# Performance work log

Measured on AMD Instinct MI355X. Metric: run time of the kernel, lower is better.

Reference implementation:

```python
import jax, jax.numpy as jnp
from jax import lax
import numpy as np
import math


def make_kernel():
    # StyleGAN2 blur kernel [1,3,3,1], normalized outer product
    k = jnp.array([1.0, 3.0, 3.0, 1.0], dtype=jnp.float32)
    k2 = jnp.outer(k, k)
    return k2 / jnp.sum(k2)


def upfirdn2d(x, kernel, up=1, pad=(0, 0)):
    # x: [B,C,H,W]; depthwise FIR filter, optional zero-insert upsampling
    C = x.shape[1]
    w = jnp.tile(jnp.flip(kernel)[None, None].astype(x.dtype), (C, 1, 1, 1))
    # torch upfirdn pads up-1 trailing zeros after the last sample; lhs_dilation
    # only inserts zeros between samples, so fold the extra zeros into pad[1].
    p = (pad[0], pad[1] + up - 1)
    return lax.conv_general_dilated(
        x, w, (1, 1), (p, p), lhs_dilation=(up, up), feature_group_count=C)


def modulated_conv(x, weight, style, demodulate=True, up=False):
    # per-sample weight modulation + demodulation, executed as grouped conv
    B, Cin, H, W = x.shape
    Cout, _, k, _ = weight.shape
    scale = 1.0 / math.sqrt(Cin * k * k)
    w = scale * weight[None] * style[:, None, :, None, None]  # [B,Cout,Cin,k,k]
    if demodulate:
        d = lax.rsqrt(jnp.sum(w * w, axis=(2, 3, 4)) + 1e-8)
        w = w * d[:, :, None, None, None]
    xg = x.reshape(1, B * Cin, H, W)
    if up:
        # conv_transpose2d(stride=2, pad=0) == lhs-dilated conv with flipped kernel
        wg = jnp.flip(w, (-2, -1)).reshape(B * Cout, Cin, k, k)
        out = lax.conv_general_dilated(
            xg, wg, (1, 1), ((k - 1, k - 1), (k - 1, k - 1)),
            lhs_dilation=(2, 2), feature_group_count=B)
    else:
        pad = k // 2
        out = lax.conv_general_dilated(
            xg, w.reshape(B * Cout, Cin, k, k), (1, 1),
            ((pad, pad), (pad, pad)), feature_group_count=B)
    return out.reshape(B, Cout, out.shape[2], out.shape[3])


def fused_lrelu(x, bias):
    y = x + bias[None, :, None, None]
    return jnp.where(y >= 0, y, 0.2 * y) * math.sqrt(2.0)


def setup_inputs() -> dict:
    key = jax.random.key(0)
    ks = jax.random.split(key, 12)
    B, C, H = 8, 512, 32
    f = jnp.float32
    return {
        "x": jax.random.normal(ks[0], (B, C, H, H), f),
        "skip": jax.random.normal(ks[1], (B, 3, H, H), f),
        "w1": jax.random.normal(ks[2], (C, C, 3, 3), f),
        "b1": jnp.zeros((C,), f),
        "s1": jax.random.normal(ks[3], (B, C), f),
        "nw1": jax.random.normal(ks[4], (1,), f) * 0.1,
        "n1": jax.random.normal(ks[5], (B, 1, 2 * H, 2 * H), f),
        "w2": jax.random.normal(ks[6], (C, C, 3, 3), f),
        "b2": jnp.zeros((C,), f),
        "s2": jax.random.normal(ks[7], (B, C), f),
        "nw2": jax.random.normal(ks[8], (1,), f) * 0.1,
        "n2": jax.random.normal(ks[9], (B, 1, 2 * H, 2 * H), f),
        "w_rgb": jax.random.normal(ks[10], (3, C, 1, 1), f),
        "b_rgb": jnp.zeros((3,), f),
        "s_rgb": jax.random.normal(ks[11], (B, C), f),
    }


def reference(x, skip, w1, b1, s1, nw1, n1, w2, b2, s2, nw2, n2,
              w_rgb, b_rgb, s_rgb):
    kern = make_kernel()
    # conv1: upsampling modulated conv + blur (Blur with upsample_factor=2)
    out = modulated_conv(x, w1, s1, demodulate=True, up=True)
    out = upfirdn2d(out, kern * 4.0, up=1, pad=(1, 1))
    out = out + nw1 * n1          # NoiseInjection
    out = fused_lrelu(out, b1)    # FusedLeakyReLU
    # conv2: plain modulated conv
    out = modulated_conv(out, w2, s2, demodulate=True)
    out = out + nw2 * n2
    out = fused_lrelu(out, b2)
    # ToRGB: 1x1 mod conv, no demodulation, + bias; skip = rgb + upsample(skip)
    rgb = modulated_conv(out, w_rgb, s_rgb, demodulate=False)
    rgb = rgb + b_rgb[None, :, None, None]
    skip_up = upfirdn2d(skip, kern * 4.0, up=2, pad=(2, 1))
    return rgb + skip_up
```

## Files before the change

### kernel.cpp

```cpp
#include <hip/hip_runtime.h>
#include <stdint.h>

typedef unsigned short ushort_t;
typedef unsigned int uint_t;
typedef __bf16 bf16x8 __attribute__((ext_vector_type(8)));
typedef float f32x4 __attribute__((ext_vector_type(4)));

#define GLOBAL_AS __attribute__((address_space(1)))
#define LDS_AS    __attribute__((address_space(3)))

#define SCALE_CONV 0.014731391f
#define SCALE_RGB  0.044194174f
#define SQRT2_F    1.41421356237f

__device__ __forceinline__ void async_cp16(const void* g, void* l) {
  __builtin_amdgcn_global_load_lds((const GLOBAL_AS uint_t*)g,
                                   (LDS_AS uint_t*)l, 16, 0, 0);
}
__device__ __forceinline__ ushort_t f2bf(float v) {
  union { float f; uint_t u; } c; c.f = v;
  uint_t r = c.u + 0x7fffu + ((c.u >> 16) & 1u);
  return (ushort_t)(r >> 16);
}
__device__ __forceinline__ float bf2f(ushort_t u) {
  union { uint_t u; float f; } c; c.u = ((uint_t)u) << 16;
  return c.f;
}

__global__ __launch_bounds__(256) void prep_x1(
    const float* __restrict__ x, const float* __restrict__ s1,
    ushort_t* __restrict__ xpad) {
  __shared__ ushort_t t[32 * 520];
  const int b  = blockIdx.x >> 5;
  const int j1 = blockIdx.x & 31;
  for (int idx = threadIdx.x; idx < 512 * 32; idx += 256) {
    int ci = idx >> 5, j2 = idx & 31;
    float v = x[(size_t)(b * 512 + ci) * 1024 + j1 * 32 + j2];
    v *= s1[b * 512 + ci] * SCALE_CONV;
    t[j2 * 520 + ci] = f2bf(v);
  }
  __syncthreads();
  for (int idx = threadIdx.x; idx < 32 * 512; idx += 256) {
    int j2 = idx >> 9, ci = idx & 511;
    xpad[((size_t)(b * 34 + j1 + 1) * 34 + (j2 + 1)) * 512 + ci] = t[j2 * 520 + ci];
  }
}

__global__ __launch_bounds__(256) void prep_w(
    const float* __restrict__ w1, const float* __restrict__ w2,
    ushort_t* __restrict__ wt1, ushort_t* __restrict__ wt2,
    float* __restrict__ wsqT1, float* __restrict__ wsqT2) {
  int t = blockIdx.x * 256 + threadIdx.x;
  const float* w  = (t < 262144) ? w1 : w2;
  ushort_t*   wt  = (t < 262144) ? wt1 : wt2;
  float*      wq  = (t < 262144) ? wsqT1 : wsqT2;
  int tt = t & 262143;
  int ci = tt & 511, co = tt >> 9;
  const float* wp = w + (size_t)(co * 512 + ci) * 9;
  float sq = 0.f;
#pragma unroll
  for (int u = 0; u < 9; ++u) {
    float v = wp[u];
    sq += v * v;
    wt[((size_t)u * 512 + co) * 512 + ci] = f2bf(v);
  }
  wq[ci * 512 + co] = sq;
}

__global__ __launch_bounds__(512) void demod2(
    const float* __restrict__ wsqT1, const float* __restrict__ s1, float* __restrict__ d1,
    const float* __restrict__ wsqT2, const float* __restrict__ s2, float* __restrict__ d2) {
  const float* wq = blockIdx.y ? wsqT2 : wsqT1;
  const float* s  = blockIdx.y ? s2 : s1;
  float*       d  = blockIdx.y ? d2 : d1;
  const int b  = blockIdx.x;
  const int co = threadIdx.x;
  __shared__ float ssq[512];
  float sv = s[b * 512 + co];
  ssq[co] = sv * sv;
  __syncthreads();
  float a = 0.f;
#pragma unroll 4
  for (int ci = 0; ci < 512; ++ci) a += wq[ci * 512 + co] * ssq[ci];
  d[b * 512 + co] = rsqrtf(a * (1.f / 4608.f) + 1e-8f);
}

__global__ __launch_bounds__(256) void border_zero(
    ushort_t* __restrict__ xpad, ushort_t* __restrict__ ypad, ushort_t* __restrict__ opad) {
  const int z = blockIdx.z;
  ushort_t* p = (z == 0) ? xpad : (z == 1 ? ypad : opad);
  const int W = (z == 0) ? 34 : (z == 1 ? 67 : 66);
  const int nb = 4 * W - 4;
  const int t = blockIdx.x * 256 + threadIdx.x;
  const int pix = t >> 6, ch = (t & 63) * 8;
  if (pix >= nb) return;
  const int b = blockIdx.y;
  int y, x;
  if (pix < W)          { y = 0;     x = pix; }
  else if (pix < 2 * W) { y = W - 1; x = pix - W; }
  else { int q = pix - 2 * W; y = 1 + (q >> 1); x = (q & 1) ? W - 1 : 0; }
  uint4 z4 = {0, 0, 0, 0};
  *(uint4*)(p + ((size_t)(b * W + y) * W + x) * 512 + ch) = z4;
}

__constant__ int           c_ph_off[4]  = {0, 4, 6, 8};
__constant__ int           c_ph_ntap[4] = {4, 2, 2, 1};
__constant__ unsigned char c_tap_u1[9]  = {0,0,1,1, 0,1, 1,1, 1};
__constant__ unsigned char c_tap_u2[9]  = {0,1,0,1, 1,1, 0,1, 1};
__constant__ unsigned char c_tap_pl[9]  = {8,6,2,0, 7,1, 5,3, 4};

__global__ __launch_bounds__(256, 3) void gemm_conv1(
    const ushort_t* __restrict__ inp, const ushort_t* __restrict__ wt,
    const float* __restrict__ dmod, ushort_t* __restrict__ outp) {
  __shared__ ushort_t ldsA[128 * 64];
  __shared__ ushort_t ldsB[128 * 64];

  const int tid  = threadIdx.x;
  const int lane = tid & 63;
  const int wv   = tid >> 6;
  const int wm   = wv & 1;
  const int wn   = wv >> 1;
  const int l16  = lane & 15;
  const int quad = lane >> 4;

  const int mtile = blockIdx.x;
  const int ntile = blockIdx.y;
  const int a  = blockIdx.z;
  const int a1 = a >> 1, a2 = a & 1;

  const int cl = ((lane & 7) - (lane >> 3)) & 7;
  const char* pA[4];
  const char* pB[4];
#pragma unroll
  for (int t = 0; t < 4; ++t) {
    int row = wv * 32 + t * 8 + (lane >> 3);
    int m   = mtile * 128 + row;
    if (m > 8711) m = 8711;
    int b = m / 1089, rr = m % 1089;
    int p1 = rr / 33, p2 = rr % 33;
    size_t pix = ((size_t)(b * 34 + p1) * 34 + p2) * 512;
    pA[t] = (const char*)inp + pix * 2 + cl * 16;
    int n = ntile * 128 + row;
    pB[t] = (const char*)wt + (size_t)n * 1024 + cl * 16;
  }
  char* dstA[4];
  char* dstB[4];
#pragma unroll
  for (int t = 0; t < 4; ++t) {
    dstA[t] = (char*)ldsA + wv * 4096 + t * 1024;
    dstB[t] = (char*)ldsB + wv * 4096 + t * 1024;
  }

  int offA[4], offB[4];
#pragma unroll
  for (int i = 0; i < 4; ++i) {
    int r  = wm * 64 + i * 16 + l16;
    int rn = wn * 64 + i * 16 + l16;
    offA[i] = r  * 64 + (((quad + r)  & 7) << 3);
    offB[i] = rn * 64 + (((quad + rn) & 7) << 3);
  }

  f32x4 acc[4][4];
#pragma unroll
  for (int i = 0; i < 4; ++i)
#pragma unroll
    for (int j = 0; j < 4; ++j) acc[i][j] = (f32x4){0.f, 0.f, 0.f, 0.f};

  const int ntap = c_ph_ntap[a];
#pragma unroll 1
  for (int ti = 0; ti < ntap; ++ti) {
    int e = c_ph_off[a] + ti;
    int aoff = ((int)c_tap_u1[e] * 34 + (int)c_tap_u2[e]) * 1024;
    int boff = (int)c_tap_pl[e] * 524288;
#pragma unroll 1
    for (int kc = 0; kc < 8; ++kc) {
      const int koff = kc * 128;
      __syncthreads();
#pragma unroll
      for (int t = 0; t < 4; ++t) async_cp16(pA[t] + aoff + koff, dstA[t]);
#pragma unroll
      for (int t = 0; t < 4; ++t) async_cp16(pB[t] + boff + koff, dstB[t]);
      __syncthreads();
#pragma unroll
      for (int kk = 0; kk < 2; ++kk) {
        const int kx = kk << 5;
        bf16x8 af[4], bg[4];
#pragma unroll
        for (int i = 0; i < 4; ++i) af[i] = *reinterpret_cast<const bf16x8*>(ldsA + (offA[i] ^ kx));
#pragma unroll
        for (int j = 0; j < 4; ++j) bg[j] = *reinterpret_cast<const bf16x8*>(ldsB + (offB[j] ^ kx));
#pragma unroll
        for (int i = 0; i < 4; ++i)
#pragma unroll
          for (int j = 0; j < 4; ++j)
            acc[i][j] = __builtin_amdgcn_mfma_f32_16x16x32_bf16(af[i], bg[j], acc[i][j], 0, 0, 0);
      }
    }
  }

  int co_[4];
#pragma unroll
  for (int j = 0; j < 4; ++j) co_[j] = ntile * 128 + wn * 64 + j * 16 + l16;

#pragma unroll
  for (int i = 0; i < 4; ++i) {
#pragma unroll
    for (int r = 0; r < 4; ++r) {
      int m = mtile * 128 + wm * 64 + i * 16 + quad * 4 + r;
      if (m < 8712) {
        int b = m / 1089, rr = m % 1089;
        int p1 = rr / 33, p2 = rr % 33;
        if ((a1 == 0 || p1 < 32) && (a2 == 0 || p2 < 32)) {
          int o1 = 2 * p1 + a1, o2 = 2 * p2 + a2;
          size_t ob = ((size_t)(b * 67 + o1 + 1) * 67 + (o2 + 1)) * 512;
#pragma unroll
          for (int j = 0; j < 4; ++j)
            outp[ob + co_[j]] = f2bf(acc[i][j][r] * dmod[b * 512 + co_[j]]);
        }
      }
    }
  }
}

__global__ __launch_bounds__(256, 2) void gemm_conv2_pipe(
    const ushort_t* __restrict__ inp, const ushort_t* __restrict__ wt,
    const float* __restrict__ dmod, const float* __restrict__ noise,
    const float* __restrict__ nw, const float* __restrict__ bias,
    const float* __restrict__ snext, float snext_scale,
    ushort_t* __restrict__ outp) {
  __shared__ ushort_t ldsA[2 * 128 * 64];
  __shared__ ushort_t ldsB[2 * 128 * 64];

  const int tid  = threadIdx.x;
  const int lane = tid & 63;
  const int wv   = tid >> 6;
  const int wm   = wv & 1;
  const int wn   = wv >> 1;
  const int l16  = lane & 15;
  const int quad = lane >> 4;

  const int mtile = blockIdx.x;
  const int ntile = blockIdx.y;

  const int cl = ((lane & 7) - (lane >> 3)) & 7;
  const char* pA[4];
  const char* pB[4];
#pragma unroll
  for (int t = 0; t < 4; ++t) {
    int row = wv * 32 + t * 8 + (lane >> 3);
    int m   = mtile * 128 + row;
    int b = m >> 12, o1 = (m >> 6) & 63, o2 = m & 63;
    size_t pix = ((size_t)(b * 66 + o1 + 1) * 66 + (o2 + 1)) * 512;
    pA[t] = (const char*)inp + pix * 2 + cl * 16;
    int n = ntile * 128 + row;
    pB[t] = (const char*)wt + (size_t)n * 1024 + cl * 16;
  }

  int offA[4], offB[4];
#pragma unroll
  for (int i = 0; i < 4; ++i) {
    int r  = wm * 64 + i * 16 + l16;
    int rn = wn * 64 + i * 16 + l16;
    offA[i] = r  * 64 + (((quad + r)  & 7) << 3);
    offB[i] = rn * 64 + (((quad + rn) & 7) << 3);
  }

  f32x4 acc[4][4];
#pragma unroll
  for (int i = 0; i < 4; ++i)
#pragma unroll
    for (int j = 0; j < 4; ++j) acc[i][j] = (f32x4){0.f, 0.f, 0.f, 0.f};

  auto stagef = [&](int k, int sel) {
    int tap = k >> 3, kc = k & 7;
    int ty = tap * 86 >> 8;
    int tx = tap - ty * 3;
    int aoff = ((ty - 1) * 66 + (tx - 1)) * 1024 + kc * 128;
    int boff = tap * 524288 + kc * 128;
    char* dA = (char*)ldsA + sel * 16384 + wv * 4096;
    char* dB = (char*)ldsB + sel * 16384 + wv * 4096;
#pragma unroll
    for (int t = 0; t < 4; ++t) async_cp16(pA[t] + aoff, dA + t * 1024);
#pragma unroll
    for (int t = 0; t < 4; ++t) async_cp16(pB[t] + boff, dB + t * 1024);
  };

  stagef(0, 0);
#pragma unroll 1
  for (int k = 0; k < 72; ++k) {
    asm volatile("s_barrier" ::: "memory");
    if (k < 71) {
      stagef(k + 1, (k + 1) & 1);
      asm volatile("s_waitcnt vmcnt(8)" ::: "memory");
    } else {
      asm volatile("s_waitcnt vmcnt(0)" ::: "memory");
    }
    asm volatile("s_barrier" ::: "memory");
    const ushort_t* bA = ldsA + (k & 1) * 8192;
    const ushort_t* bB = ldsB + (k & 1) * 8192;
#pragma unroll
    for (int kk = 0; kk < 2; ++kk) {
      const int kx = kk << 5;
      bf16x8 af[4], bg[4];
#pragma unroll
      for (int i = 0; i < 4; ++i) af[i] = *reinterpret_cast<const bf16x8*>(bA + (offA[i] ^ kx));
#pragma unroll
      for (int j = 0; j < 4; ++j) bg[j] = *reinterpret_cast<const bf16x8*>(bB + (offB[j] ^ kx));
#pragma unroll
      for (int i = 0; i < 4; ++i)
#pragma unroll
        for (int j = 0; j < 4; ++j)
          acc[i][j] = __builtin_amdgcn_mfma_f32_16x16x32_bf16(af[i], bg[j], acc[i][j], 0, 0, 0);
    }
  }

  const int b = mtile >> 5;
  int co_[4];
#pragma unroll
  for (int j = 0; j < 4; ++j) co_[j] = ntile * 128 + wn * 64 + j * 16 + l16;
  const float nwv = nw[0];
  float dj_[4], sj_[4], bj_[4];
#pragma unroll
  for (int j = 0; j < 4; ++j) {
    dj_[j] = dmod[b * 512 + co_[j]];
    sj_[j] = snext[b * 512 + co_[j]] * snext_scale;
    bj_[j] = bias[co_[j]];
  }
#pragma unroll
  for (int i = 0; i < 4; ++i) {
#pragma unroll
    for (int r = 0; r < 4; ++r) {
      int m = mtile * 128 + wm * 64 + i * 16 + quad * 4 + r;
      int o1 = (m >> 6) & 63, o2 = m & 63;
      float nz = nwv * noise[(b << 12) + (o1 << 6) + o2];
      size_t ob = ((size_t)(b * 64 + o1) * 64 + o2) * 512;
#pragma unroll
      for (int j = 0; j < 4; ++j) {
        float v = acc[i][j][r] * dj_[j] + nz + bj_[j];
        v = (v >= 0.f ? v : 0.2f * v) * SQRT2_F;
        v *= sj_[j];
        outp[ob + co_[j]] = f2bf(v);
      }
    }
  }
}

__global__ __launch_bounds__(256) void blur_noise_act(
    const ushort_t* __restrict__ y1pad, const float* __restrict__ noise,
    const float* __restrict__ nw, const float* __restrict__ bias,
    const float* __restrict__ s2, ushort_t* __restrict__ out1pad) {
  const int cg  = threadIdx.x & 63;
  const int pg  = blockIdx.x * 4 + (threadIdx.x >> 6);
  const int b   = pg >> 10;
  const int q1  = (pg >> 4) & 63;
  const int q2g = (pg & 15) * 4;
  const float cw[4] = {0.25f, 0.75f, 0.75f, 0.25f};

  float acc[4][8];
#pragma unroll
  for (int j = 0; j < 4; ++j)
#pragma unroll
    for (int e = 0; e < 8; ++e) acc[j][e] = 0.f;

#pragma unroll
  for (int t2 = 0; t2 < 7; ++t2) {
    int cc = q2g + t2;
    float vt[8];
#pragma unroll
    for (int e = 0; e < 8; ++e) vt[e] = 0.f;
#pragma unroll
    for (int t1 = 0; t1 < 4; ++t1) {
      const ushort_t* p = y1pad + ((size_t)(b * 67 + q1 + t1) * 67 + cc) * 512 + cg * 8;
      ushort_t v[8];
      *(uint4*)v = *(const uint4*)p;
#pragma unroll
      for (int e = 0; e < 8; ++e) vt[e] += cw[t1] * bf2f(v[e]);
    }
#pragma unroll
    for (int j = 0; j < 4; ++j) {
      int t = t2 - j;
      if (t >= 0 && t < 4) {
#pragma unroll
        for (int e = 0; e < 8; ++e) acc[j][e] += cw[t] * vt[e];
      }
    }
  }

  const float nwv = nw[0];
  float bj[8], sj[8];
#pragma unroll
  for (int e = 0; e < 8; ++e) {
    bj[e] = bias[cg * 8 + e];
    sj[e] = s2[b * 512 + cg * 8 + e] * SCALE_CONV;
  }
#pragma unroll
  for (int j = 0; j < 4; ++j) {
    int q2 = q2g + j;
    float nz = nwv * noise[(b << 12) + (q1 << 6) + q2];
    ushort_t o[8];
#pragma unroll
    for (int e = 0; e < 8; ++e) {
      float v = acc[j][e] + nz + bj[e];
      v = (v >= 0.f ? v : 0.2f * v) * SQRT2_F * sj[e];
      o[e] = f2bf(v);
    }
    *(uint4*)(out1pad + ((size_t)(b * 66 + q1 + 1) * 66 + (q2 + 1)) * 512 + cg * 8) = *(uint4*)o;
  }
}

__global__ __launch_bounds__(256) void torgb_skip(
    const ushort_t* __restrict__ out2s, const float* __restrict__ wrgb,
    const float* __restrict__ brgb, const float* __restrict__ skip,
    float* __restrict__ out) {
  const int lane = threadIdx.x & 63;
  const int pix  = blockIdx.x * 4 + (threadIdx.x >> 6);
  const int b = pix >> 12, o1 = (pix >> 6) & 63, o2 = pix & 63;
  const ushort_t* src = out2s + (size_t)pix * 512 + lane * 8;
  ushort_t v[8];
  *(uint4*)v = *(const uint4*)src;
  float s0 = 0.f, s1 = 0.f, s2 = 0.f;
#pragma unroll
  for (int e = 0; e < 8; ++e) {
    float xv = bf2f(v[e]);
    int ci = lane * 8 + e;
    s0 += xv * wrgb[ci];
    s1 += xv * wrgb[512 + ci];
    s2 += xv * wrgb[1024 + ci];
  }
#pragma unroll
  for (int o = 32; o; o >>= 1) {
    s0 += __shfl_xor(s0, o);
    s1 += __shfl_xor(s1, o);
    s2 += __shfl_xor(s2, o);
  }
  if (lane < 3) {
    float v3 = (lane == 0) ? s0 : (lane == 1 ? s1 : s2);
    int P1 = o1 >> 1, P2 = o2 >> 1;
    int jy0, jy1, jx0, jx1;
    float wy0, wy1, wx0, wx1;
    if ((o1 & 1) == 0) { jy0 = P1 - 1; wy0 = .25f; jy1 = P1;     wy1 = .75f; }
    else               { jy0 = P1;     wy0 = .75f; jy1 = P1 + 1; wy1 = .25f; }
    if ((o2 & 1) == 0) { jx0 = P2 - 1; wx0 = .25f; jx1 = P2;     wx1 = .75f; }
    else               { jx0 = P2;     wx0 = .75f; jx1 = P2 + 1; wx1 = .25f; }
    const float* sp = skip + (size_t)(b * 3 + lane) * 1024;
    float sv = 0.f;
    if (jy0 >= 0 && jy0 < 32) {
      if (jx0 >= 0 && jx0 < 32) sv += wy0 * wx0 * sp[jy0 * 32 + jx0];
      if (jx1 >= 0 && jx1 < 32) sv += wy0 * wx1 * sp[jy0 * 32 + jx1];
    }
    if (jy1 >= 0 && jy1 < 32) {
      if (jx0 >= 0 && jx0 < 32) sv += wy1 * wx0 * sp[jy1 * 32 + jx0];
      if (jx1 >= 0 && jx1 < 32) sv += wy1 * wx1 * sp[jy1 * 32 + jx1];
    }
    out[((size_t)(b * 3 + lane) << 12) + (o1 << 6) + o2] = v3 + brgb[lane] + sv;
  }
}

extern "C" void kernel_launch(void* const* d_in, const int* in_sizes, int n_in,
                              void* d_out, int out_size, void* d_ws, size_t ws_size,
                              hipStream_t stream) {
  const float* x    = (const float*)d_in[0];
  const float* skip = (const float*)d_in[1];
  const float* w1   = (const float*)d_in[2];
  const float* b1   = (const float*)d_in[3];
  const float* s1   = (const float*)d_in[4];
  const float* nw1  = (const float*)d_in[5];
  const float* n1   = (const float*)d_in[6];
  const float* w2   = (const float*)d_in[7];
  const float* b2   = (const float*)d_in[8];
  const float* s2   = (const float*)d_in[9];
  const float* nw2  = (const float*)d_in[10];
  const float* n2   = (const float*)d_in[11];
  const float* wrgb = (const float*)d_in[12];
  const float* brgb = (const float*)d_in[13];
  const float* srgb = (const float*)d_in[14];

  char* ws = (char*)d_ws;
  const size_t XPAD_B  = (size_t)8 * 34 * 34 * 512 * 2;
  const size_t Y1PAD_B = (size_t)8 * 67 * 67 * 512 * 2;
  const size_t OUT1_B  = (size_t)8 * 66 * 66 * 512 * 2;
  const size_t WT_B    = (size_t)9 * 512 * 512 * 2;
  size_t off = 0;
  ushort_t* xpad1   = (ushort_t*)(ws + off); off += XPAD_B;
  ushort_t* y1pad   = (ushort_t*)(ws + off); off += Y1PAD_B;
  ushort_t* out1pad = (ushort_t*)(ws + off); off += OUT1_B;
  ushort_t* wt1     = (ushort_t*)(ws + off); off += WT_B;
  ushort_t* wt2     = (ushort_t*)(ws + off); off += WT_B;
  float*    d1      = (float*)(ws + off);    off += 8 * 512 * 4;
  float*    d2      = (float*)(ws + off);    off += 8 * 512 * 4;
  ushort_t* out2s  = y1pad;
  float*    wsqT1  = (float*)y1pad;
  float*    wsqT2  = wsqT1 + 512 * 512;

  prep_x1<<<256, 256, 0, stream>>>(x, s1, xpad1);
  prep_w<<<2048, 256, 0, stream>>>(w1, w2, wt1, wt2, wsqT1, wsqT2);
  demod2<<<dim3(8, 2), 512, 0, stream>>>(wsqT1, s1, d1, wsqT2, s2, d2);
  border_zero<<<dim3(66, 8, 3), 256, 0, stream>>>(xpad1, y1pad, out1pad);

  gemm_conv1<<<dim3(69, 4, 4), 256, 0, stream>>>(xpad1, wt1, d1, y1pad);
  blur_noise_act<<<2048, 256, 0, stream>>>(y1pad, n1, nw1, b1, s2, out1pad);
  gemm_conv2_pipe<<<dim3(256, 4), 256, 0, stream>>>(
      out1pad, wt2, d2, n2, nw2, b2, srgb, SCALE_RGB, out2s);
  torgb_skip<<<8192, 256, 0, stream>>>(out2s, wrgb, brgb, skip, (float*)d_out);
}
```

Before: 407.0 us.

## Fuse ToRGB projection into conv2 epilogue with atomics; drop double buffering

The conv2 GEMM epilogue now does the 1x1 ToRGB projection itself. Each wave reduces its 64 channels per pixel with shuffles and atomically adds partial RGB sums into a small fp32 buffer. This removes the bf16 write and re-read of the full 512-channel conv2 output. A lightweight kernel then adds bias and the upsampled skip. The conv2 K-loop also goes from double-buffered async staging to single-buffered with two syncthreads per step, and occupancy hints are raised to 4 for both GEMMs. This trades load/compute overlap for more resident blocks, and adds a memset plus atomic contention.

```diff
diff --git a/kernel.cpp b/kernel.cpp
--- a/kernel.cpp
+++ b/kernel.cpp
@@ -109,7 +109,7 @@
 __constant__ unsigned char c_tap_u2[9]  = {0,1,0,1, 1,1, 0,1, 1};
 __constant__ unsigned char c_tap_pl[9]  = {8,6,2,0, 7,1, 5,3, 4};
 
-__global__ __launch_bounds__(256, 3) void gemm_conv1(
+__global__ __launch_bounds__(256, 4) void gemm_conv1(
     const ushort_t* __restrict__ inp, const ushort_t* __restrict__ wt,
     const float* __restrict__ dmod, ushort_t* __restrict__ outp) {
   __shared__ ushort_t ldsA[128 * 64];
@@ -222,14 +222,14 @@
   }
 }
 
-__global__ __launch_bounds__(256, 2) void gemm_conv2_pipe(
+__global__ __launch_bounds__(256, 4) void gemm_conv2(
     const ushort_t* __restrict__ inp, const ushort_t* __restrict__ wt,
     const float* __restrict__ dmod, const float* __restrict__ noise,
     const float* __restrict__ nw, const float* __restrict__ bias,
-    const float* __restrict__ snext, float snext_scale,
-    ushort_t* __restrict__ outp) {
-  __shared__ ushort_t ldsA[2 * 128 * 64];
-  __shared__ ushort_t ldsB[2 * 128 * 64];
+    const float* __restrict__ srgb, const float* __restrict__ wrgb,
+    float* __restrict__ rgbpart) {
+  __shared__ ushort_t ldsA[128 * 64];
+  __shared__ ushort_t ldsB[128 * 64];
 
   const int tid  = threadIdx.x;
   const int lane = tid & 63;
@@ -255,6 +255,13 @@
     int n = ntile * 128 + row;
     pB[t] = (const char*)wt + (size_t)n * 1024 + cl * 16;
   }
+  char* dstA[4];
+  char* dstB[4];
+#pragma unroll
+  for (int t = 0; t < 4; ++t) {
+    dstA[t] = (char*)ldsA + wv * 4096 + t * 1024;
+    dstB[t] = (char*)ldsB + wv * 4096 + t * 1024;
+  }
 
   int offA[4], offB[4];
 #pragma unroll
@@ -271,46 +278,33 @@
 #pragma unroll
     for (int j = 0; j < 4; ++j) acc[i][j] = (f32x4){0.f, 0.f, 0.f, 0.f};
 
-  auto stagef = [&](int k, int sel) {
-    int tap = k >> 3, kc = k & 7;
-    int ty = tap * 86 >> 8;
-    int tx = tap - ty * 3;
-    int aoff = ((ty - 1) * 66 + (tx - 1)) * 1024 + kc * 128;
-    int boff = tap * 524288 + kc * 128;
-    char* dA = (char*)ldsA + sel * 16384 + wv * 4096;
-    char* dB = (char*)ldsB + sel * 16384 + wv * 4096;
-#pragma unroll
-    for (int t = 0; t < 4; ++t) async_cp16(pA[t] + aoff, dA + t * 1024);
-#pragma unroll
-    for (int t = 0; t < 4; ++t) async_cp16(pB[t] + boff, dB + t * 1024);
-  };
-
-  stagef(0, 0);
 #pragma unroll 1
-  for (int k = 0; k < 72; ++k) {
-    asm volatile("s_barrier" ::: "memory");
-    if (k < 71) {
-      stagef(k + 1, (k + 1) & 1);
-      asm volatile("s_waitcnt vmcnt(8)" ::: "memory");
-    } else {
-      asm volatile("s_waitcnt vmcnt(0)" ::: "memory");
-    }
-    asm volatile("s_barrier" ::: "memory");
-    const ushort_t* bA = ldsA + (k & 1) * 8192;
-    const ushort_t* bB = ldsB + (k & 1) * 8192;
-#pragma unroll
-    for (int kk = 0; kk < 2; ++kk) {
-      const int kx = kk << 5;
-      bf16x8 af[4], bg[4];
-#pragma unroll
-      for (int i = 0; i < 4; ++i) af[i] = *reinterpret_cast<const bf16x8*>(bA + (offA[i] ^ kx));
-#pragma unroll
-      for (int j = 0; j < 4; ++j) bg[j] = *reinterpret_cast<const bf16x8*>(bB + (offB[j] ^ kx));
-#pragma unroll
-      for (int i = 0; i < 4; ++i)
-#pragma unroll
-        for (int j = 0; j < 4; ++j)
-          acc[i][j] = __builtin_amdgcn_mfma_f32_16x16x32_bf16(af[i], bg[j], acc[i][j], 0, 0, 0);
+  for (int ti = 0; ti < 9; ++ti) {
+    int aoff = ((ti / 3 - 1) * 66 + (ti % 3 - 1)) * 1024;
+    int boff = ti * 524288;
+#pragma unroll 1
+    for (int kc = 0; kc < 8; ++kc) {
+      const int koff = kc * 128;
+      __syncthreads();
+#pragma unroll
+      for (int t = 0; t < 4; ++t) async_cp16(pA[t] + aoff + koff, dstA[t]);
+#pragma unroll
+      for (int t = 0; t < 4; ++t) async_cp16(pB[t] + boff + koff, dstB[t]);
+      __syncthreads();
+#pragma unroll
+      for (int kk = 0; kk < 2; ++kk) {
+        const int kx = kk << 5;
+        bf16x8 af[4], bg[4];
+#pragma unroll
+        for (int i = 0; i < 4; ++i) af[i] = *reinterpret_cast<const bf16x8*>(ldsA + (offA[i] ^ kx));
+#pragma unroll
+        for (int j = 0; j < 4; ++j) bg[j] = *reinterpret_cast<const bf16x8*>(ldsB + (offB[j] ^ kx));
+#pragma unroll
+        for (int i = 0; i < 4; ++i)
+#pragma unroll
+          for (int j = 0; j < 4; ++j)
+            acc[i][j] = __builtin_amdgcn_mfma_f32_16x16x32_bf16(af[i], bg[j], acc[i][j], 0, 0, 0);
+      }
     }
   }
 
@@ -319,12 +313,14 @@
 #pragma unroll
   for (int j = 0; j < 4; ++j) co_[j] = ntile * 128 + wn * 64 + j * 16 + l16;
   const float nwv = nw[0];
-  float dj_[4], sj_[4], bj_[4];
+  float dj_[4], sj_[4], bj_[4], wr[3][4];
 #pragma unroll
   for (int j = 0; j < 4; ++j) {
     dj_[j] = dmod[b * 512 + co_[j]];
-    sj_[j] = snext[b * 512 + co_[j]] * snext_scale;
+    sj_[j] = srgb[b * 512 + co_[j]] * SCALE_RGB;
     bj_[j] = bias[co_[j]];
+#pragma unroll
+    for (int c = 0; c < 3; ++c) wr[c][j] = wrgb[c * 512 + co_[j]];
   }
 #pragma unroll
   for (int i = 0; i < 4; ++i) {
@@ -333,13 +329,21 @@
       int m = mtile * 128 + wm * 64 + i * 16 + quad * 4 + r;
       int o1 = (m >> 6) & 63, o2 = m & 63;
       float nz = nwv * noise[(b << 12) + (o1 << 6) + o2];
-      size_t ob = ((size_t)(b * 64 + o1) * 64 + o2) * 512;
+      float vv[4];
 #pragma unroll
       for (int j = 0; j < 4; ++j) {
         float v = acc[i][j][r] * dj_[j] + nz + bj_[j];
         v = (v >= 0.f ? v : 0.2f * v) * SQRT2_F;
-        v *= sj_[j];
-        outp[ob + co_[j]] = f2bf(v);
+        vv[j] = v * sj_[j];
+      }
+#pragma unroll
+      for (int c = 0; c < 3; ++c) {
+        float s = vv[0] * wr[c][0] + vv[1] * wr[c][1] + vv[2] * wr[c][2] + vv[3] * wr[c][3];
+        s += __shfl_xor(s, 1);
+        s += __shfl_xor(s, 2);
+        s += __shfl_xor(s, 4);
+        s += __shfl_xor(s, 8);
+        if (l16 == 0) atomicAdd(&rgbpart[c * 32768 + m], s);
       }
     }
   }
@@ -408,52 +412,31 @@
   }
 }
 
-__global__ __launch_bounds__(256) void torgb_skip(
-    const ushort_t* __restrict__ out2s, const float* __restrict__ wrgb,
-    const float* __restrict__ brgb, const float* __restrict__ skip,
-    float* __restrict__ out) {
-  const int lane = threadIdx.x & 63;
-  const int pix  = blockIdx.x * 4 + (threadIdx.x >> 6);
-  const int b = pix >> 12, o1 = (pix >> 6) & 63, o2 = pix & 63;
-  const ushort_t* src = out2s + (size_t)pix * 512 + lane * 8;
-  ushort_t v[8];
-  *(uint4*)v = *(const uint4*)src;
-  float s0 = 0.f, s1 = 0.f, s2 = 0.f;
-#pragma unroll
-  for (int e = 0; e < 8; ++e) {
-    float xv = bf2f(v[e]);
-    int ci = lane * 8 + e;
-    s0 += xv * wrgb[ci];
-    s1 += xv * wrgb[512 + ci];
-    s2 += xv * wrgb[1024 + ci];
-  }
-#pragma unroll
-  for (int o = 32; o; o >>= 1) {
-    s0 += __shfl_xor(s0, o);
-    s1 += __shfl_xor(s1, o);
-    s2 += __shfl_xor(s2, o);
-  }
-  if (lane < 3) {
-    float v3 = (lane == 0) ? s0 : (lane == 1 ? s1 : s2);
-    int P1 = o1 >> 1, P2 = o2 >> 1;
-    int jy0, jy1, jx0, jx1;
-    float wy0, wy1, wx0, wx1;
-    if ((o1 & 1) == 0) { jy0 = P1 - 1; wy0 = .25f; jy1 = P1;     wy1 = .75f; }
-    else               { jy0 = P1;     wy0 = .75f; jy1 = P1 + 1; wy1 = .25f; }
-    if ((o2 & 1) == 0) { jx0 = P2 - 1; wx0 = .25f; jx1 = P2;     wx1 = .75f; }
-    else               { jx0 = P2;     wx0 = .75f; jx1 = P2 + 1; wx1 = .25f; }
-    const float* sp = skip + (size_t)(b * 3 + lane) * 1024;
-    float sv = 0.f;
-    if (jy0 >= 0 && jy0 < 32) {
-      if (jx0 >= 0 && jx0 < 32) sv += wy0 * wx0 * sp[jy0 * 32 + jx0];
-      if (jx1 >= 0 && jx1 < 32) sv += wy0 * wx1 * sp[jy0 * 32 + jx1];
-    }
-    if (jy1 >= 0 && jy1 < 32) {
-      if (jx0 >= 0 && jx0 < 32) sv += wy1 * wx0 * sp[jy1 * 32 + jx0];
-      if (jx1 >= 0 && jx1 < 32) sv += wy1 * wx1 * sp[jy1 * 32 + jx1];
-    }
-    out[((size_t)(b * 3 + lane) << 12) + (o1 << 6) + o2] = v3 + brgb[lane] + sv;
-  }
+__global__ __launch_bounds__(256) void rgb_finish(
+    const float* __restrict__ rgbpart, const float* __restrict__ brgb,
+    const float* __restrict__ skip, float* __restrict__ out) {
+  const int t = blockIdx.x * 256 + threadIdx.x;
+  if (t >= 98304) return;
+  const int m = t & 32767, c = t >> 15;
+  const int b = m >> 12, o1 = (m >> 6) & 63, o2 = m & 63;
+  int P1 = o1 >> 1, P2 = o2 >> 1;
+  int jy0, jy1, jx0, jx1;
+  float wy0, wy1, wx0, wx1;
+  if ((o1 & 1) == 0) { jy0 = P1 - 1; wy0 = .25f; jy1 = P1;     wy1 = .75f; }
+  else               { jy0 = P1;     wy0 = .75f; jy1 = P1 + 1; wy1 = .25f; }
+  if ((o2 & 1) == 0) { jx0 = P2 - 1; wx0 = .25f; jx1 = P2;     wx1 = .75f; }
+  else               { jx0 = P2;     wx0 = .75f; jx1 = P2 + 1; wx1 = .25f; }
+  const float* sp = skip + (size_t)(b * 3 + c) * 1024;
+  float sv = 0.f;
+  if (jy0 >= 0 && jy0 < 32) {
+    if (jx0 >= 0 && jx0 < 32) sv += wy0 * wx0 * sp[jy0 * 32 + jx0];
+    if (jx1 >= 0 && jx1 < 32) sv += wy0 * wx1 * sp[jy0 * 32 + jx1];
+  }
+  if (jy1 >= 0 && jy1 < 32) {
+    if (jx0 >= 0 && jx0 < 32) sv += wy1 * wx0 * sp[jy1 * 32 + jx0];
+    if (jx1 >= 0 && jx1 < 32) sv += wy1 * wx1 * sp[jy1 * 32 + jx1];
+  }
+  out[((size_t)(b * 3 + c) << 12) + (o1 << 6) + o2] = rgbpart[c * 32768 + m] + brgb[c] + sv;
 }
 
 extern "C" void kernel_launch(void* const* d_in, const int* in_sizes, int n_in,
@@ -488,10 +471,11 @@
   ushort_t* wt2     = (ushort_t*)(ws + off); off += WT_B;
   float*    d1      = (float*)(ws + off);    off += 8 * 512 * 4;
   float*    d2      = (float*)(ws + off);    off += 8 * 512 * 4;
-  ushort_t* out2s  = y1pad;
+  float*    rgbpart = (float*)(ws + off);    off += 3 * 32768 * 4;
   float*    wsqT1  = (float*)y1pad;
   float*    wsqT2  = wsqT1 + 512 * 512;
 
+  hipMemsetAsync(rgbpart, 0, 3 * 32768 * 4, stream);
   prep_x1<<<256, 256, 0, stream>>>(x, s1, xpad1);
   prep_w<<<2048, 256, 0, stream>>>(w1, w2, wt1, wt2, wsqT1, wsqT2);
   demod2<<<dim3(8, 2), 512, 0, stream>>>(wsqT1, s1, d1, wsqT2, s2, d2);
@@ -499,7 +483,7 @@
 
   gemm_conv1<<<dim3(69, 4, 4), 256, 0, stream>>>(xpad1, wt1, d1, y1pad);
   blur_noise_act<<<2048, 256, 0, stream>>>(y1pad, n1, nw1, b1, s2, out1pad);
-  gemm_conv2_pipe<<<dim3(256, 4), 256, 0, stream>>>(
-      out1pad, wt2, d2, n2, nw2, b2, srgb, SCALE_RGB, out2s);
-  torgb_skip<<<8192, 256, 0, stream>>>(out2s, wrgb, brgb, skip, (float*)d_out);
-}
+  gemm_conv2<<<dim3(256, 4), 256, 0, stream>>>(
+      out1pad, wt2, d2, n2, nw2, b2, srgb, wrgb, rgbpart);
+  rgb_finish<<<384, 256, 0, stream>>>(rgbpart, brgb, skip, (float*)d_out);
+}
```

After: 392.1 us. -3.7%, faster.
